# Kernel tuning notes

Measured on AMD Instinct MI355X. Metric: run time of the kernel, lower is better.

The kernel has to match this reference:

```python
import jax, jax.numpy as jnp
import numpy as np

B, C, H, W = 32, 512, 64, 64
RED = 16
HID = C // RED


def setup_inputs() -> dict:
    key = jax.random.key(0)
    ks = jax.random.split(key, 10)
    s1 = 1.0 / np.sqrt(C)
    s2 = 1.0 / np.sqrt(HID)
    return {
        "x": jax.random.normal(ks[0], (B, C, H, W), dtype=jnp.float32),
        # mlp_avg: Linear(C->HID), Linear(HID->C); torch convention W:[out,in]
        "Wa1": jax.random.uniform(ks[1], (HID, C), jnp.float32, -s1, s1),
        "ba1": jax.random.uniform(ks[2], (HID,), jnp.float32, -s1, s1),
        "Wa2": jax.random.uniform(ks[3], (C, HID), jnp.float32, -s2, s2),
        "ba2": jax.random.uniform(ks[4], (C,), jnp.float32, -s2, s2),
        # mlp_max
        "Wm1": jax.random.uniform(ks[5], (HID, C), jnp.float32, -s1, s1),
        "bm1": jax.random.uniform(ks[6], (HID,), jnp.float32, -s1, s1),
        "Wm2": jax.random.uniform(ks[7], (C, HID), jnp.float32, -s2, s2),
        "bm2": jax.random.uniform(ks[8], (C,), jnp.float32, -s2, s2),
        "fusion_w": jax.random.normal(ks[9], (5, 1), dtype=jnp.float32),
    }


def reference(x, Wa1, ba1, Wa2, ba2, Wm1, bm1, Wm2, bm2, fusion_w):
    b, c, h, w = x.shape
    hs, ws = h // 2, w // 2

    def mlp(v, W1, b1, W2, b2):  # v: [..., c]
        return jax.nn.relu(v @ W1.T + b1) @ W2.T + b2

    # quadrant view: [b, c, 2, hs, 2, ws]; quadrant (i,j) == x[:,:,i*hs:(i+1)*hs, j*ws:(j+1)*ws]
    xq = x.reshape(b, c, 2, hs, 2, ws)
    avg_q = xq.mean(axis=(3, 5))          # [b, c, 2, 2]
    max_q = xq.max(axis=(3, 5))           # [b, c, 2, 2]
    avg_g = x.mean(axis=(2, 3))           # [b, c]
    max_g = x.max(axis=(2, 3))            # [b, c]

    # stack regions in order [global, x1=(0,0), x2=(0,1), x3=(1,0), x4=(1,1)] -> [5, b, c]
    avg_all = jnp.concatenate(
        [avg_g[None], avg_q.transpose(2, 3, 0, 1).reshape(4, b, c)], axis=0)
    max_all = jnp.concatenate(
        [max_g[None], max_q.transpose(2, 3, 0, 1).reshape(4, b, c)], axis=0)

    feats = mlp(avg_all, Wa1, ba1, Wa2, ba2) + mlp(max_all, Wm1, bm1, Wm2, bm2)  # [5, b, c]

    fw = jax.nn.softmax(fusion_w[:, 0], axis=0)          # [5]
    fused = jnp.einsum('sbc,s->bc', feats, fw)           # [b, c]

    global_att = jax.nn.sigmoid(fused)                   # [b, c]
    local_att = jax.nn.sigmoid(feats[1:])                # [4, b, c] (x1..x4)
    scale = local_att + global_att[None]                 # [4, b, c]

    # scatter per-quadrant scale back into [b, c, 2, 1, 2, 1] and multiply
    s = scale.reshape(2, 2, b, c).transpose(2, 3, 0, 1)[:, :, :, None, :, None]
    out = (xq * s).reshape(b, c, h, w)
    return out
```

## Files before the change

### kernel.cpp

```cpp
#include <hip/hip_runtime.h>
#include <math.h>

#define Bn  32
#define Cn  512
#define HIDn 32
#define BCn (Bn*Cn)

typedef float f32x4 __attribute__((ext_vector_type(4)));

__global__ __launch_bounds__(256) void stats_kernel(const float* __restrict__ x,
                                                    float* __restrict__ avg_all,
                                                    float* __restrict__ max_all) {
  const int wave = threadIdx.x >> 6;
  const int lane = threadIdx.x & 63;
  const int plane = blockIdx.x * 4 + wave;
  const f32x4* xp = (const f32x4*)(x + (size_t)plane * 4096);

  float sT = 0.f, sB = 0.f, mT = -INFINITY, mB = -INFINITY;
#pragma unroll
  for (int i = 0; i < 16; ++i) {
    f32x4 v = xp[lane + 64 * i];
    float s = (v.x + v.y) + (v.z + v.w);
    float m = fmaxf(fmaxf(v.x, v.y), fmaxf(v.z, v.w));
    if (i < 8) { sT += s; mT = fmaxf(mT, m); }
    else       { sB += s; mB = fmaxf(mB, m); }
  }

  const int masks[5] = {1, 2, 4, 16, 32};
#pragma unroll
  for (int t = 0; t < 5; ++t) {
    const int msk = masks[t];
    sT += __shfl_xor(sT, msk);
    sB += __shfl_xor(sB, msk);
    mT = fmaxf(mT, __shfl_xor(mT, msk));
    mB = fmaxf(mB, __shfl_xor(mB, msk));
  }
  const float sTo = __shfl_xor(sT, 8), sBo = __shfl_xor(sB, 8);
  const float mTo = __shfl_xor(mT, 8), mBo = __shfl_xor(mB, 8);

  if (lane == 0) {
    avg_all[1 * BCn + plane] = sT  * (1.f / 1024.f);
    avg_all[2 * BCn + plane] = sTo * (1.f / 1024.f);
    avg_all[3 * BCn + plane] = sB  * (1.f / 1024.f);
    avg_all[4 * BCn + plane] = sBo * (1.f / 1024.f);
    avg_all[plane]           = (sT + sTo + sB + sBo) * (1.f / 4096.f);
    max_all[1 * BCn + plane] = mT;
    max_all[2 * BCn + plane] = mTo;
    max_all[3 * BCn + plane] = mB;
    max_all[4 * BCn + plane] = mBo;
    max_all[plane]           = fmaxf(fmaxf(mT, mTo), fmaxf(mB, mBo));
  }
}

__global__ __launch_bounds__(256) void mlp_kernel(
    const float* __restrict__ avg_all, const float* __restrict__ max_all,
    const float* __restrict__ Wa1, const float* __restrict__ ba1,
    const float* __restrict__ Wa2, const float* __restrict__ ba2,
    const float* __restrict__ Wm1, const float* __restrict__ bm1,
    const float* __restrict__ Wm2, const float* __restrict__ bm2,
    const float* __restrict__ fusion_w, float* __restrict__ scale_ws) {
  const int b = blockIdx.x;
  const int tid = threadIdx.x;

  __shared__ __align__(16) float s_v[2][5][Cn];
  __shared__ float s_h[2][5][HIDn];

  for (int i = tid; i < 5 * Cn; i += 256) {
    int s = i >> 9, c = i & (Cn - 1);
    s_v[0][s][c] = avg_all[s * BCn + b * Cn + c];
    s_v[1][s][c] = max_all[s * BCn + b * Cn + c];
  }
  __syncthreads();

  for (int d = tid; d < 2 * 5 * HIDn; d += 256) {
    int mlp = d / 160, r = d % 160;
    int s = r >> 5, k = r & 31;
    const float* W1 = mlp ? Wm1 : Wa1;
    const float* b1 = mlp ? bm1 : ba1;
    const f32x4* wrow = (const f32x4*)(W1 + k * Cn);
    const f32x4* v = (const f32x4*)s_v[mlp][s];
    float acc = b1[k];
    for (int c4 = 0; c4 < Cn / 4; ++c4) {
      f32x4 w = wrow[c4], xv = v[c4];
      acc += w.x * xv.x + w.y * xv.y + w.z * xv.z + w.w * xv.w;
    }
    s_h[mlp][s][k] = fmaxf(acc, 0.f);
  }
  __syncthreads();

  float fw[5]; float fmx = -INFINITY;
#pragma unroll
  for (int s = 0; s < 5; ++s) { fw[s] = fusion_w[s]; fmx = fmaxf(fmx, fw[s]); }
  float fsum = 0.f;
#pragma unroll
  for (int s = 0; s < 5; ++s) { fw[s] = expf(fw[s] - fmx); fsum += fw[s]; }
  const float finv = 1.f / fsum;

  {
    const int c = blockIdx.y * 256 + tid;
    const float* wa = Wa2 + c * HIDn;
    const float* wm = Wm2 + c * HIDn;
    const float bias = ba2[c] + bm2[c];
    float f[5];
#pragma unroll
    for (int s = 0; s < 5; ++s) {
      float acc = bias;
#pragma unroll
      for (int k = 0; k < HIDn; ++k)
        acc += wa[k] * s_h[0][s][k] + wm[k] * s_h[1][s][k];
      f[s] = acc;
    }
    float fused = 0.f;
#pragma unroll
    for (int s = 0; s < 5; ++s) fused += fw[s] * f[s];
    fused *= finv;
    const float g = 1.f / (1.f + expf(-fused));
    float4 sc;
    sc.x = 1.f / (1.f + expf(-f[1])) + g;
    sc.y = 1.f / (1.f + expf(-f[2])) + g;
    sc.z = 1.f / (1.f + expf(-f[3])) + g;
    sc.w = 1.f / (1.f + expf(-f[4])) + g;
    ((float4*)scale_ws)[b * Cn + c] = sc;
  }
}

__global__ __launch_bounds__(256) void apply_kernel(const float* __restrict__ x,
                                                    const float* __restrict__ scale_ws,
                                                    float* __restrict__ out) {
  const int wave = threadIdx.x >> 6;
  const int lane = threadIdx.x & 63;
  const int plane = blockIdx.x * 4 + wave;
  const int jside = ((lane & 15) >= 8) ? 1 : 0;

  const float scT = scale_ws[plane * 4 + jside];
  const float scB = scale_ws[plane * 4 + 2 + jside];

  const f32x4* xp = (const f32x4*)(x + (size_t)plane * 4096);
  f32x4* op = (f32x4*)(out + (size_t)plane * 4096);

#pragma unroll
  for (int i = 0; i < 16; ++i) {
    f32x4 v = xp[lane + 64 * i];
    v *= (i < 8) ? scT : scB;
    __builtin_nontemporal_store(v, &op[lane + 64 * i]);
  }
}

extern "C" void kernel_launch(void* const* d_in, const int* in_sizes, int n_in,
                              void* d_out, int out_size, void* d_ws, size_t ws_size,
                              hipStream_t stream) {
  const float* x        = (const float*)d_in[0];
  const float* Wa1      = (const float*)d_in[1];
  const float* ba1      = (const float*)d_in[2];
  const float* Wa2      = (const float*)d_in[3];
  const float* ba2      = (const float*)d_in[4];
  const float* Wm1      = (const float*)d_in[5];
  const float* bm1      = (const float*)d_in[6];
  const float* Wm2      = (const float*)d_in[7];
  const float* bm2      = (const float*)d_in[8];
  const float* fusion_w = (const float*)d_in[9];
  float* out = (float*)d_out;

  float* ws       = (float*)d_ws;
  float* avg_all  = ws;
  float* max_all  = ws + 5 * BCn;
  float* scale_ws = ws + 10 * BCn;

  stats_kernel<<<BCn / 4, 256, 0, stream>>>(x, avg_all, max_all);
  mlp_kernel<<<dim3(Bn, 2), 256, 0, stream>>>(avg_all, max_all,
                                              Wa1, ba1, Wa2, ba2,
                                              Wm1, bm1, Wm2, bm2,
                                              fusion_w, scale_ws);
  apply_kernel<<<BCn / 4, 256, 0, stream>>>(x, scale_ws, out);
}
```

Before: 159.8 us.

## Fuse MLP attention computation into the apply kernel, recomputing hidden layer per block

Merges the MLP kernel and the apply kernel into one launch. Each block handles 16 planes of one batch: it recomputes the first MLP layer (320 dot products of length 512) from global stats, computes the second layer only for its 16 channels, then scales x. This removes a kernel launch and the scale workspace round trip. In exchange the first MLP layer is recomputed redundantly by 32 blocks per batch, adding latency before each block starts streaming x.

```diff
diff --git a/kernel.cpp b/kernel.cpp
--- a/kernel.cpp
+++ b/kernel.cpp
@@ -5,6 +5,7 @@
 #define Cn  512
 #define HIDn 32
 #define BCn (Bn*Cn)
+#define PPB 16
 
 typedef float f32x4 __attribute__((ext_vector_type(4)));
 
@@ -52,33 +53,31 @@
   }
 }
 
-__global__ __launch_bounds__(256) void mlp_kernel(
+__global__ __launch_bounds__(256) void fused_apply_kernel(
+    const float* __restrict__ x,
     const float* __restrict__ avg_all, const float* __restrict__ max_all,
     const float* __restrict__ Wa1, const float* __restrict__ ba1,
     const float* __restrict__ Wa2, const float* __restrict__ ba2,
     const float* __restrict__ Wm1, const float* __restrict__ bm1,
     const float* __restrict__ Wm2, const float* __restrict__ bm2,
-    const float* __restrict__ fusion_w, float* __restrict__ scale_ws) {
-  const int b = blockIdx.x;
+    const float* __restrict__ fusion_w,
+    float* __restrict__ out) {
   const int tid = threadIdx.x;
+  const int b   = blockIdx.x >> 5;
+  const int c0  = (blockIdx.x & 31) * PPB;
 
-  __shared__ __align__(16) float s_v[2][5][Cn];
   __shared__ float s_h[2][5][HIDn];
-
-  for (int i = tid; i < 5 * Cn; i += 256) {
-    int s = i >> 9, c = i & (Cn - 1);
-    s_v[0][s][c] = avg_all[s * BCn + b * Cn + c];
-    s_v[1][s][c] = max_all[s * BCn + b * Cn + c];
-  }
-  __syncthreads();
+  __shared__ float s_f[PPB][5];
+  __shared__ float s_scale[PPB][4];
 
   for (int d = tid; d < 2 * 5 * HIDn; d += 256) {
-    int mlp = d / 160, r = d % 160;
-    int s = r >> 5, k = r & 31;
+    const int mlp = d / 160, r = d % 160;
+    const int s = r >> 5, k = r & 31;
     const float* W1 = mlp ? Wm1 : Wa1;
     const float* b1 = mlp ? bm1 : ba1;
+    const float* stat = (mlp ? max_all : avg_all) + s * BCn + b * Cn;
     const f32x4* wrow = (const f32x4*)(W1 + k * Cn);
-    const f32x4* v = (const f32x4*)s_v[mlp][s];
+    const f32x4* v = (const f32x4*)stat;
     float acc = b1[k];
     for (int c4 = 0; c4 < Cn / 4; ++c4) {
       f32x4 w = wrow[c4], xv = v[c4];
@@ -88,61 +87,56 @@
   }
   __syncthreads();
 
-  float fw[5]; float fmx = -INFINITY;
-#pragma unroll
-  for (int s = 0; s < 5; ++s) { fw[s] = fusion_w[s]; fmx = fmaxf(fmx, fw[s]); }
-  float fsum = 0.f;
-#pragma unroll
-  for (int s = 0; s < 5; ++s) { fw[s] = expf(fw[s] - fmx); fsum += fw[s]; }
-  const float finv = 1.f / fsum;
-
-  {
-    const int c = blockIdx.y * 256 + tid;
+  if (tid < PPB * 5) {
+    const int cl = tid / 5, s = tid % 5;
+    const int c = c0 + cl;
     const float* wa = Wa2 + c * HIDn;
     const float* wm = Wm2 + c * HIDn;
-    const float bias = ba2[c] + bm2[c];
-    float f[5];
+    float acc = ba2[c] + bm2[c];
 #pragma unroll
-    for (int s = 0; s < 5; ++s) {
-      float acc = bias;
+    for (int k = 0; k < HIDn; ++k)
+      acc += wa[k] * s_h[0][s][k] + wm[k] * s_h[1][s][k];
+    s_f[cl][s] = acc;
+  }
+  __syncthreads();
+
+  if (tid < PPB) {
+    float fw[5]; float fmx = -INFINITY;
 #pragma unroll
-      for (int k = 0; k < HIDn; ++k)
-        acc += wa[k] * s_h[0][s][k] + wm[k] * s_h[1][s][k];
-      f[s] = acc;
-    }
+    for (int s = 0; s < 5; ++s) { fw[s] = fusion_w[s]; fmx = fmaxf(fmx, fw[s]); }
+    float fsum = 0.f;
+#pragma unroll
+    for (int s = 0; s < 5; ++s) { fw[s] = expf(fw[s] - fmx); fsum += fw[s]; }
     float fused = 0.f;
 #pragma unroll
-    for (int s = 0; s < 5; ++s) fused += fw[s] * f[s];
-    fused *= finv;
+    for (int s = 0; s < 5; ++s) fused += fw[s] * s_f[tid][s];
+    fused /= fsum;
     const float g = 1.f / (1.f + expf(-fused));
-    float4 sc;
-    sc.x = 1.f / (1.f + expf(-f[1])) + g;
-    sc.y = 1.f / (1.f + expf(-f[2])) + g;
-    sc.z = 1.f / (1.f + expf(-f[3])) + g;
-    sc.w = 1.f / (1.f + expf(-f[4])) + g;
-    ((float4*)scale_ws)[b * Cn + c] = sc;
+    s_scale[tid][0] = 1.f / (1.f + expf(-s_f[tid][1])) + g;
+    s_scale[tid][1] = 1.f / (1.f + expf(-s_f[tid][2])) + g;
+    s_scale[tid][2] = 1.f / (1.f + expf(-s_f[tid][3])) + g;
+    s_scale[tid][3] = 1.f / (1.f + expf(-s_f[tid][4])) + g;
   }
-}
+  __syncthreads();
 
-__global__ __launch_bounds__(256) void apply_kernel(const float* __restrict__ x,
-                                                    const float* __restrict__ scale_ws,
-                                                    float* __restrict__ out) {
-  const int wave = threadIdx.x >> 6;
-  const int lane = threadIdx.x & 63;
-  const int plane = blockIdx.x * 4 + wave;
+  const int wave = tid >> 6;
+  const int lane = tid & 63;
   const int jside = ((lane & 15) >= 8) ? 1 : 0;
 
-  const float scT = scale_ws[plane * 4 + jside];
-  const float scB = scale_ws[plane * 4 + 2 + jside];
-
-  const f32x4* xp = (const f32x4*)(x + (size_t)plane * 4096);
-  f32x4* op = (f32x4*)(out + (size_t)plane * 4096);
-
 #pragma unroll
-  for (int i = 0; i < 16; ++i) {
-    f32x4 v = xp[lane + 64 * i];
-    v *= (i < 8) ? scT : scB;
-    __builtin_nontemporal_store(v, &op[lane + 64 * i]);
+  for (int q = 0; q < 4; ++q) {
+    const int p_loc = wave * 4 + q;
+    const int plane = blockIdx.x * PPB + p_loc;
+    const float scT = s_scale[p_loc][jside];
+    const float scB = s_scale[p_loc][2 + jside];
+    const f32x4* xp = (const f32x4*)(x + (size_t)plane * 4096);
+    f32x4* op = (f32x4*)(out + (size_t)plane * 4096);
+#pragma unroll
+    for (int i = 0; i < 16; ++i) {
+      f32x4 v = xp[lane + 64 * i];
+      v *= (i < 8) ? scT : scB;
+      __builtin_nontemporal_store(v, &op[lane + 64 * i]);
+    }
   }
 }
 
@@ -164,12 +158,10 @@
   float* ws       = (float*)d_ws;
   float* avg_all  = ws;
   float* max_all  = ws + 5 * BCn;
-  float* scale_ws = ws + 10 * BCn;
 
   stats_kernel<<<BCn / 4, 256, 0, stream>>>(x, avg_all, max_all);
-  mlp_kernel<<<dim3(Bn, 2), 256, 0, stream>>>(avg_all, max_all,
-                                              Wa1, ba1, Wa2, ba2,
-                                              Wm1, bm1, Wm2, bm2,
-                                              fusion_w, scale_ws);
-  apply_kernel<<<BCn / 4, 256, 0, stream>>>(x, scale_ws, out);
+  fused_apply_kernel<<<BCn / PPB, 256, 0, stream>>>(x, avg_all, max_all,
+                                                    Wa1, ba1, Wa2, ba2,
+                                                    Wm1, bm1, Wm2, bm2,
+                                                    fusion_w, out);
 }
```

Result: slower. 202.2 us (+26.6%).
